# Performance work log

Measured on AMD Instinct MI355X. Metric: run time of the kernel, lower is better.

## Reference

```python
import jax, jax.numpy as jnp
import numpy as np

C = 112       # channels, divisible by NCHUNK
NCHUNK = 7    # shift_sizes[0]
PAD = 3       # shift_sizes[0] // 2
EPS = 1e-5


def _gn(x, g, b):
    # GroupNorm(1, C): normalize over (C, D, H, W) per sample, per-channel affine
    mu = jnp.mean(x, axis=(1, 2, 3, 4), keepdims=True)
    var = jnp.mean((x - mu) ** 2, axis=(1, 2, 3, 4), keepdims=True)
    xn = (x - mu) * jax.lax.rsqrt(var + EPS)
    return xn * g[None, :, None, None, None] + b[None, :, None, None, None]


def _conv1x1(x, w, b):
    # 1x1x1 Conv3d == channel-mixing GEMM
    return jnp.einsum('oc,bcdhw->bodhw', w, x) + b[None, :, None, None, None]


def _gelu(x):
    return jax.nn.gelu(x, approximate=False)  # torch nn.GELU default = exact erf


def _pad3(x):
    return jnp.pad(x, ((0, 0), (0, 0), (PAD, PAD), (PAD, PAD), (PAD, PAD)))


def _axial_shift(xp, axis, D, H, W):
    # chunk channels into NCHUNK groups, roll group i by (i - PAD) along `axis`,
    # concat, then narrow each spatial axis at offset PAD with ORIGINAL lengths
    chunks = jnp.split(xp, NCHUNK, axis=1)
    shifted = [jnp.roll(c, s, axis=axis) for c, s in zip(chunks, range(-PAD, PAD + 1))]
    xc = jnp.concatenate(shifted, axis=1)
    return xc[:, :, PAD:PAD + D, PAD:PAD + H, PAD:PAD + W]


def setup_inputs() -> dict:
    key = jax.random.key(0)
    ks = jax.random.split(key, 9)
    B, D, H, W = 1, 64, 64, 64
    hid = 4 * C

    def w(k, shape, fan_in):
        return jax.random.normal(k, shape, jnp.float32) * np.float32(1.0 / np.sqrt(fan_in))

    return {
        'x': jax.random.normal(ks[0], (B, C, D, H, W), jnp.float32),
        'conv1_w': w(ks[1], (C, C), C), 'conv1_b': jnp.zeros((C,), jnp.float32),
        'conv2d_w': w(ks[2], (C, C), C), 'conv2d_b': jnp.zeros((C,), jnp.float32),
        'conv2h_w': w(ks[3], (C, C), C), 'conv2h_b': jnp.zeros((C,), jnp.float32),
        'conv2w_w': w(ks[4], (C, C), C), 'conv2w_b': jnp.zeros((C,), jnp.float32),
        'conv3_w': w(ks[5], (C, C), C), 'conv3_b': jnp.zeros((C,), jnp.float32),
        'fc1_w': w(ks[6], (hid, C), C), 'fc1_b': jnp.zeros((hid,), jnp.float32),
        'fc2_w': w(ks[7], (C, hid), hid), 'fc2_b': jnp.zeros((C,), jnp.float32),
        'n1_g': jnp.ones((C,), jnp.float32), 'n1_b': jnp.zeros((C,), jnp.float32),
        'na1_g': jnp.ones((C,), jnp.float32), 'na1_b': jnp.zeros((C,), jnp.float32),
        'na2_g': jnp.ones((C,), jnp.float32), 'na2_b': jnp.zeros((C,), jnp.float32),
        'n2_g': jnp.ones((C,), jnp.float32), 'n2_b': jnp.zeros((C,), jnp.float32),
    }


def reference(x, conv1_w, conv1_b, conv2d_w, conv2d_b, conv2h_w, conv2h_b,
              conv2w_w, conv2w_b, conv3_w, conv3_b, fc1_w, fc1_b, fc2_w, fc2_b,
              n1_g, n1_b, na1_g, na1_b, na2_g, na2_b, n2_g, n2_b):
    B, _, D, H, W = x.shape
    shortcut = x
    h0 = _gn(x, n1_g, n1_b)                                   # block norm1

    # ---- AxialShift.axial_shift_single_scale ----
    a = _gelu(_gn(_conv1x1(h0, conv1_w, conv1_b), na1_g, na1_b))
    xp = _pad3(a)                                             # padded once (D branch)
    x_d = _gelu(_conv1x1(_axial_shift(xp, 2, D, H, W), conv2d_w, conv2d_b))
    xp = _pad3(xp)                                            # padded twice (H branch, as in source)
    x_h = _gelu(_conv1x1(_axial_shift(xp, 3, D, H, W), conv2h_w, conv2h_b))
    xp = _pad3(xp)                                            # padded thrice (W branch)
    x_w = _gelu(_conv1x1(_axial_shift(xp, 4, D, H, W), conv2w_w, conv2w_b))
    y = _conv1x1(_gn(x_d + x_h + x_w, na2_g, na2_b), conv3_w, conv3_b)
    y = y + h0                                                # AxialShift residual (x_masked == 0)

    x1 = shortcut + y                                         # block residual 1
    m = _gn(x1, n2_g, n2_b)                                   # block norm2
    m = _conv1x1(_gelu(_conv1x1(m, fc1_w, fc1_b)), fc2_w, fc2_b)  # Mlp (drop=0)
    return x1 + m
```

## Files before the change

### kernel.cpp

```cpp
#include <hip/hip_runtime.h>
#include <math.h>

static constexpr int CH   = 112;
static constexpr int HID  = 448;
static constexpr int NPOS = 64 * 64 * 64;
static constexpr long long NELEM = (long long)CH * NPOS;

typedef _Float16 f16x8 __attribute__((ext_vector_type(8)));
typedef _Float16 f16x4 __attribute__((ext_vector_type(4)));
typedef float    f32x4 __attribute__((ext_vector_type(4)));

__device__ __forceinline__ float gelu_f(float x) {
    return 0.5f * x * (1.0f + erff(x * 0.70710678118654752f));
}

__device__ __forceinline__ void stats_from(const double* __restrict__ S, float* mu, float* inv) {
    double m = S[0] / (double)NELEM;
    double v = S[1] / (double)NELEM - m * m;
    *mu  = (float)m;
    *inv = (float)(1.0 / sqrt(v + 1e-5));
}

__device__ __forceinline__ void block_reduce2(double s, double q, double* __restrict__ out) {
    #pragma unroll
    for (int off = 32; off > 0; off >>= 1) {
        s += __shfl_down(s, off, 64);
        q += __shfl_down(q, off, 64);
    }
    __shared__ double red[16];
    int lane = threadIdx.x & 63, wv = threadIdx.x >> 6;
    int nw = blockDim.x >> 6;
    if (lane == 0) { red[wv] = s; red[wv + 8] = q; }
    __syncthreads();
    if (threadIdx.x == 0) {
        double S = 0, Q = 0;
        for (int i = 0; i < nw; i++) { S += red[i]; Q += red[i + 8]; }
        atomicAdd(out, S);
        atomicAdd(out + 1, Q);
    }
}

__device__ __forceinline__ void mfma_tile(const _Float16* __restrict__ w,
                                          const _Float16 (*lsT)[136],
                                          int l15, int l4, int wv, f32x4 acc[7]) {
    #pragma unroll
    for (int kk = 0; kk < 4; kk++) {
        f16x8 b = *(const f16x8*)(&lsT[wv * 16 + l15][kk * 32 + l4 * 8]);
        #pragma unroll
        for (int mt = 0; mt < 7; mt++) {
            f16x8 a = *(const f16x8*)(w + (mt * 16 + l15) * 128 + kk * 32 + l4 * 8);
            acc[mt] = __builtin_amdgcn_mfma_f32_16x16x32_f16(a, b, acc[mt], 0, 0, 0);
        }
    }
}

__device__ __forceinline__ void accum_gelu(f32x4 tot[7], const f32x4 acc[7],
                                           const float* __restrict__ b, int l4) {
    #pragma unroll
    for (int mt = 0; mt < 7; mt++) {
        float4 bb = *(const float4*)(b + mt * 16 + l4 * 4);
        tot[mt][0] += gelu_f(acc[mt][0] + bb.x);
        tot[mt][1] += gelu_f(acc[mt][1] + bb.y);
        tot[mt][2] += gelu_f(acc[mt][2] + bb.z);
        tot[mt][3] += gelu_f(acc[mt][3] + bb.w);
    }
}

__global__ void k_reduce(const float* __restrict__ x, double* __restrict__ S) {
    long long i0 = (long long)blockIdx.x * blockDim.x + threadIdx.x;
    long long stride = (long long)gridDim.x * blockDim.x;
    const float4* x4 = (const float4*)x;
    long long n4 = NELEM / 4;
    double s = 0, q = 0;
    for (long long i = i0; i < n4; i += stride) {
        float4 v = x4[i];
        s += (double)v.x + (double)v.y + (double)v.z + (double)v.w;
        q += (double)v.x * v.x + (double)v.y * v.y + (double)v.z * v.z + (double)v.w * v.w;
    }
    block_reduce2(s, q, S);
}

__global__ void k_fold(const double* __restrict__ S, const float* __restrict__ w,
                       const float* __restrict__ b, const float* __restrict__ g,
                       const float* __restrict__ bta,
                       _Float16* __restrict__ w16, float* __restrict__ beff) {
    int o = blockIdx.x;
    float mu, inv; stats_from(S, &mu, &inv);
    float partial = 0.f;
    for (int c = threadIdx.x; c < 128; c += blockDim.x) {
        float wv_ = 0.f, contrib = 0.f;
        if (c < CH) {
            float sc = inv * g[c];
            float sh = bta[c] - mu * sc;
            float w0 = w[o * CH + c];
            wv_ = w0 * sc;
            contrib = w0 * sh;
        }
        w16[o * 128 + c] = (_Float16)wv_;
        partial += contrib;
    }
    #pragma unroll
    for (int off = 32; off > 0; off >>= 1) partial += __shfl_down(partial, off, 64);
    __shared__ float rp[2];
    int lane = threadIdx.x & 63, wv_ = threadIdx.x >> 6;
    if (lane == 0) rp[wv_] = partial;
    __syncthreads();
    if (threadIdx.x == 0) beff[o] = b[o] + rp[0] + rp[1];
}

__global__ void k_cast(const float* __restrict__ w2d, const float* __restrict__ w2h,
                       const float* __restrict__ w2w, const float* __restrict__ fc2w,
                       _Float16* __restrict__ w2dh, _Float16* __restrict__ w2hh,
                       _Float16* __restrict__ w2wh, _Float16* __restrict__ fc2h) {
    int b = blockIdx.x;
    if (b < CH) {
        for (int c = threadIdx.x; c < 128; c += blockDim.x) {
            float vd = 0.f, vh = 0.f, vw = 0.f;
            if (c < CH) { vd = w2d[b * CH + c]; vh = w2h[b * CH + c]; vw = w2w[b * CH + c]; }
            w2dh[b * 128 + c] = (_Float16)vd;
            w2hh[b * 128 + c] = (_Float16)vh;
            w2wh[b * 128 + c] = (_Float16)vw;
        }
    }
    for (int i = threadIdx.x; i < CH; i += blockDim.x)
        fc2h[b * CH + i] = (_Float16)fc2w[b * CH + i];
}

__global__ void __launch_bounds__(256, 2)
k_conv1(const float* __restrict__ x, const _Float16* __restrict__ w1h,
        const float* __restrict__ b1e, _Float16* __restrict__ t16, double* __restrict__ S1) {
    __shared__ __align__(16) _Float16 lxT[64][136];
    int tid = threadIdx.x, lane = tid & 63, wv = tid >> 6, l15 = lane & 15, l4 = lane >> 4;
    int pos0 = blockIdx.x * 64;

    {
        int c0 = tid >> 4, q = tid & 15;
        #pragma unroll
        for (int p = 0; p < 7; p++) {
            int c = p * 16 + c0;
            float4 v = *(const float4*)(x + (long long)c * NPOS + pos0 + q * 4);
            lxT[q * 4 + 0][c] = (_Float16)v.x;
            lxT[q * 4 + 1][c] = (_Float16)v.y;
            lxT[q * 4 + 2][c] = (_Float16)v.z;
            lxT[q * 4 + 3][c] = (_Float16)v.w;
        }
        for (int i = tid; i < 64 * 16; i += 256) lxT[i >> 4][112 + (i & 15)] = (_Float16)0.f;
    }
    __syncthreads();

    f32x4 acc[7];
    {
        f32x4 z = {0.f, 0.f, 0.f, 0.f};
        #pragma unroll
        for (int mt = 0; mt < 7; mt++) acc[mt] = z;
    }
    mfma_tile(w1h, lxT, l15, l4, wv, acc);

    long long posw = pos0 + wv * 16 + l15;
    double s = 0, q = 0;
    #pragma unroll
    for (int mt = 0; mt < 7; mt++) {
        int ob = mt * 16 + l4 * 4;
        float4 bb = *(const float4*)(b1e + ob);
        const float* bp = (const float*)&bb;
        f16x4 o4;
        #pragma unroll
        for (int r = 0; r < 4; r++) {
            float tv = acc[mt][r] + bp[r];
            o4[r] = (_Float16)tv;
            s += (double)tv; q += (double)tv * tv;
        }
        *(f16x4*)(t16 + posw * 128 + ob) = o4;
    }
    {
        f16x4 z4; z4[0] = z4[1] = z4[2] = z4[3] = (_Float16)0.f;
        *(f16x4*)(t16 + posw * 128 + 112 + l4 * 4) = z4;
    }
    block_reduce2(s, q, S1);
}

__global__ void k_act(const _Float16* __restrict__ t16, _Float16* __restrict__ a16,
                      const double* __restrict__ S1, const float* __restrict__ g,
                      const float* __restrict__ bta) {
    float mu, inv; stats_from(S1, &mu, &inv);
    long long i8 = (long long)blockIdx.x * blockDim.x + threadIdx.x;
    int c = (int)((i8 * 8) & 127);
    f16x8 r;
    if (c < 112) {
        f16x8 v = *(const f16x8*)(t16 + i8 * 8);
        float4 g0 = *(const float4*)(g + c);
        float4 g1 = *(const float4*)(g + c + 4);
        float4 b0 = *(const float4*)(bta + c);
        float4 b1 = *(const float4*)(bta + c + 4);
        const float* gp0 = (const float*)&g0; const float* gp1 = (const float*)&g1;
        const float* bp0 = (const float*)&b0; const float* bp1 = (const float*)&b1;
        #pragma unroll
        for (int j = 0; j < 4; j++) {
            float sc = inv * gp0[j], sh = bp0[j] - mu * sc;
            r[j] = (_Float16)gelu_f((float)v[j] * sc + sh);
        }
        #pragma unroll
        for (int j = 0; j < 4; j++) {
            float sc = inv * gp1[j], sh = bp1[j] - mu * sc;
            r[4 + j] = (_Float16)gelu_f((float)v[4 + j] * sc + sh);
        }
    } else {
        #pragma unroll
        for (int j = 0; j < 8; j++) r[j] = (_Float16)0.f;
    }
    *(f16x8*)(a16 + i8 * 8) = r;
}

__global__ void __launch_bounds__(256, 2)
k_shift(const _Float16* __restrict__ a16,
        const _Float16* __restrict__ w2dh, const float* __restrict__ b2d,
        const _Float16* __restrict__ w2hh, const float* __restrict__ b2h,
        const _Float16* __restrict__ w2wh, const float* __restrict__ b2w,
        _Float16* __restrict__ s16, double* __restrict__ S2) {
    __shared__ __align__(16) _Float16 lsT[64][136];
    int tid = threadIdx.x, lane = tid & 63, wv = tid >> 6, l15 = lane & 15, l4 = lane >> 4;
    int d = blockIdx.x >> 6, h = blockIdx.x & 63;

    f32x4 tot[7], acc[7];
    {
        f32x4 z = {0.f, 0.f, 0.f, 0.f};
        #pragma unroll
        for (int mt = 0; mt < 7; mt++) tot[mt] = z;
    }
    f16x8 z8;
    #pragma unroll
    for (int j = 0; j < 8; j++) z8[j] = (_Float16)0.f;

    for (int u = tid; u < 1024; u += 256) {
        int w = u >> 4, u16 = u & 15;
        f16x8 v = z8;
        if (u16 < 14) {
            int p = u16 >> 1;
            int dd = d - (p - 3);
            if ((unsigned)dd < 64u)
                v = *(const f16x8*)(a16 + (long long)(dd * 4096 + h * 64 + w) * 128 + u16 * 8);
        }
        *(f16x8*)(&lsT[w][u16 * 8]) = v;
    }
    __syncthreads();
    {
        f32x4 z = {0.f, 0.f, 0.f, 0.f};
        #pragma unroll
        for (int mt = 0; mt < 7; mt++) acc[mt] = z;
    }
    mfma_tile(w2dh, lsT, l15, l4, wv, acc);
    accum_gelu(tot, acc, b2d, l4);
    __syncthreads();

    {
        int dd = d - 3;
        bool dok = (unsigned)dd < 64u;
        for (int u = tid; u < 1024; u += 256) {
            int w = u >> 4, u16 = u & 15;
            f16x8 v = z8;
            if (u16 < 14) {
                int p = u16 >> 1;
                int hh = h - p;
                int ww = w - 3;
                if (dok && (unsigned)hh < 64u && ww >= 0)
                    v = *(const f16x8*)(a16 + (long long)(dd * 4096 + hh * 64 + ww) * 128 + u16 * 8);
            }
            *(f16x8*)(&lsT[w][u16 * 8]) = v;
        }
    }
    __syncthreads();
    {
        f32x4 z = {0.f, 0.f, 0.f, 0.f};
        #pragma unroll
        for (int mt = 0; mt < 7; mt++) acc[mt] = z;
    }
    mfma_tile(w2hh, lsT, l15, l4, wv, acc);
    accum_gelu(tot, acc, b2h, l4);
    __syncthreads();

    {
        int dd = d - 6, hh = h - 6;
        bool ok = ((unsigned)dd < 64u) && ((unsigned)hh < 64u);
        for (int u = tid; u < 1024; u += 256) {
            int w = u >> 4, u16 = u & 15;
            f16x8 v = z8;
            if (ok && u16 < 14) {
                int p = u16 >> 1;
                int ww = w - 3 - p;
                if ((unsigned)ww < 64u)
                    v = *(const f16x8*)(a16 + (long long)(dd * 4096 + hh * 64 + ww) * 128 + u16 * 8);
            }
            *(f16x8*)(&lsT[w][u16 * 8]) = v;
        }
    }
    __syncthreads();
    {
        f32x4 z = {0.f, 0.f, 0.f, 0.f};
        #pragma unroll
        for (int mt = 0; mt < 7; mt++) acc[mt] = z;
    }
    mfma_tile(w2wh, lsT, l15, l4, wv, acc);
    accum_gelu(tot, acc, b2w, l4);

    long long posw = d * 4096 + h * 64 + wv * 16 + l15;
    double s = 0, q = 0;
    #pragma unroll
    for (int mt = 0; mt < 7; mt++) {
        f16x4 o4;
        #pragma unroll
        for (int r = 0; r < 4; r++) {
            float sv = tot[mt][r];
            o4[r] = (_Float16)sv;
            s += (double)sv; q += (double)sv * sv;
        }
        *(f16x4*)(s16 + posw * 128 + mt * 16 + l4 * 4) = o4;
    }
    {
        f16x4 z4; z4[0] = z4[1] = z4[2] = z4[3] = (_Float16)0.f;
        *(f16x4*)(s16 + posw * 128 + 112 + l4 * 4) = z4;
    }
    block_reduce2(s, q, S2);
}

__global__ void __launch_bounds__(256, 2)
k_comb(const _Float16* __restrict__ s16, const float* __restrict__ x,
       const _Float16* __restrict__ w3h, const float* __restrict__ b3e,
       const double* __restrict__ S0, const float* __restrict__ n1g,
       const float* __restrict__ n1b, float* __restrict__ x1, double* __restrict__ S3) {
    __shared__ __align__(16) _Float16 lsT[64][136];
    int tid = threadIdx.x, lane = tid & 63, wv = tid >> 6, l15 = lane & 15, l4 = lane >> 4;
    int pos0 = blockIdx.x * 64;

    for (int u = tid; u < 1024; u += 256) {
        int w = u >> 4, u16 = u & 15;
        *(f16x8*)(&lsT[w][u16 * 8]) =
            *(const f16x8*)(s16 + (long long)(pos0 + w) * 128 + u16 * 8);
    }
    __syncthreads();

    f32x4 acc[7];
    {
        f32x4 z = {0.f, 0.f, 0.f, 0.f};
        #pragma unroll
        for (int mt = 0; mt < 7; mt++) acc[mt] = z;
    }
    mfma_tile(w3h, lsT, l15, l4, wv, acc);

    float mu, inv; stats_from(S0, &mu, &inv);
    long long posw = pos0 + wv * 16 + l15;
    double s = 0, q = 0;
    #pragma unroll
    for (int mt = 0; mt < 7; mt++) {
        int ob = mt * 16 + l4 * 4;
        float4 b3 = *(const float4*)(b3e + ob);
        float4 g4 = *(const float4*)(n1g + ob);
        float4 n4 = *(const float4*)(n1b + ob);
        const float* b3p = (const float*)&b3;
        const float* g4p = (const float*)&g4;
        const float* n4p = (const float*)&n4;
        #pragma unroll
        for (int r = 0; r < 4; r++) {
            int o = ob + r;
            float y  = acc[mt][r] + b3p[r];
            float xv = x[(long long)o * NPOS + posw];
            float sc = inv * g4p[r];
            float h0 = xv * sc + (n4p[r] - mu * sc);
            float v  = xv + y + h0;
            x1[(long long)o * NPOS + posw] = v;
            s += (double)v; q += (double)v * v;
        }
    }
    block_reduce2(s, q, S3);
}

__global__ void __launch_bounds__(256, 2)
k_mlp(float* __restrict__ x1out, const _Float16* __restrict__ fc1h,
      const float* __restrict__ b1m, const _Float16* __restrict__ fc2h,
      const float* __restrict__ fc2b) {
    __shared__ __align__(16) _Float16 lxT[64][136];
    __shared__ __align__(16) _Float16 GT[64][456];
    int tid  = threadIdx.x;
    int lane = tid & 63;
    int wv   = tid >> 6;
    int l15  = lane & 15;
    int l4   = lane >> 4;
    int pos0 = blockIdx.x * 64;

    {
        int c0 = tid >> 4;
        int q  = tid & 15;
        #pragma unroll
        for (int p = 0; p < 7; p++) {
            int c = p * 16 + c0;
            float4 v = *(const float4*)(x1out + (long long)c * NPOS + pos0 + q * 4);
            lxT[q * 4 + 0][c] = (_Float16)v.x;
            lxT[q * 4 + 1][c] = (_Float16)v.y;
            lxT[q * 4 + 2][c] = (_Float16)v.z;
            lxT[q * 4 + 3][c] = (_Float16)v.w;
        }
        for (int i = tid; i < 64 * 16; i += 256) {
            lxT[i >> 4][112 + (i & 15)] = (_Float16)0.f;
        }
    }
    __syncthreads();

    int hb = wv * 112;
    f32x4 acc1[7][4];
    {
        f32x4 z = {0.f, 0.f, 0.f, 0.f};
        #pragma unroll
        for (int mt = 0; mt < 7; mt++)
            #pragma unroll
            for (int nt = 0; nt < 4; nt++) acc1[mt][nt] = z;
    }
    #pragma unroll
    for (int kk = 0; kk < 4; kk++) {
        f16x8 a[7];
        #pragma unroll
        for (int mt = 0; mt < 7; mt++)
            a[mt] = *(const f16x8*)(fc1h + (hb + mt * 16 + l15) * 128 + kk * 32 + l4 * 8);
        #pragma unroll
        for (int nt = 0; nt < 4; nt++) {
            f16x8 b = *(const f16x8*)(&lxT[nt * 16 + l15][kk * 32 + l4 * 8]);
            #pragma unroll
            for (int mt = 0; mt < 7; mt++)
                acc1[mt][nt] = __builtin_amdgcn_mfma_f32_16x16x32_f16(a[mt], b, acc1[mt][nt], 0, 0, 0);
        }
    }
    #pragma unroll
    for (int mt = 0; mt < 7; mt++) {
        int hbase = hb + mt * 16 + l4 * 4;
        float4 bias = *(const float4*)(b1m + hbase);
        #pragma unroll
        for (int nt = 0; nt < 4; nt++) {
            f16x4 g4;
            g4[0] = (_Float16)gelu_f(acc1[mt][nt][0] + bias.x);
            g4[1] = (_Float16)gelu_f(acc1[mt][nt][1] + bias.y);
            g4[2] = (_Float16)gelu_f(acc1[mt][nt][2] + bias.z);
            g4[3] = (_Float16)gelu_f(acc1[mt][nt][3] + bias.w);
            *(f16x4*)(&GT[nt * 16 + l15][hbase]) = g4;
        }
    }
    __syncthreads();

    int pw = wv * 16 + l15;
    f32x4 acc2[7];
    {
        f32x4 z = {0.f, 0.f, 0.f, 0.f};
        #pragma unroll
        for (int mt = 0; mt < 7; mt++) acc2[mt] = z;
    }
    #pragma unroll 2
    for (int kk = 0; kk < 14; kk++) {
        f16x8 b = *(const f16x8*)(&GT[pw][kk * 32 + l4 * 8]);
        #pragma unroll
        for (int mt = 0; mt < 7; mt++) {
            f16x8 a = *(const f16x8*)(fc2h + (mt * 16 + l15) * 448 + kk * 32 + l4 * 8);
            acc2[mt] = __builtin_amdgcn_mfma_f32_16x16x32_f16(a, b, acc2[mt], 0, 0, 0);
        }
    }
    long long gp = pos0 + pw;
    #pragma unroll
    for (int mt = 0; mt < 7; mt++) {
        int ob = mt * 16 + l4 * 4;
        float4 b2 = *(const float4*)(fc2b + ob);
        float bb[4] = {b2.x, b2.y, b2.z, b2.w};
        #pragma unroll
        for (int r = 0; r < 4; r++) {
            long long idx = (long long)(ob + r) * NPOS + gp;
            x1out[idx] = x1out[idx] + acc2[mt][r] + bb[r];
        }
    }
}

extern "C" void kernel_launch(void* const* d_in, const int* in_sizes, int n_in,
                              void* d_out, int out_size, void* d_ws, size_t ws_size,
                              hipStream_t stream) {
    const float* x       = (const float*)d_in[0];
    const float* conv1_w = (const float*)d_in[1];
    const float* conv1_b = (const float*)d_in[2];
    const float* conv2d_w= (const float*)d_in[3];
    const float* conv2d_b= (const float*)d_in[4];
    const float* conv2h_w= (const float*)d_in[5];
    const float* conv2h_b= (const float*)d_in[6];
    const float* conv2w_w= (const float*)d_in[7];
    const float* conv2w_b= (const float*)d_in[8];
    const float* conv3_w = (const float*)d_in[9];
    const float* conv3_b = (const float*)d_in[10];
    const float* fc1_w   = (const float*)d_in[11];
    const float* fc1_b   = (const float*)d_in[12];
    const float* fc2_w   = (const float*)d_in[13];
    const float* fc2_b   = (const float*)d_in[14];
    const float* n1_g    = (const float*)d_in[15];
    const float* n1_b    = (const float*)d_in[16];
    const float* na1_g   = (const float*)d_in[17];
    const float* na1_b   = (const float*)d_in[18];
    const float* na2_g   = (const float*)d_in[19];
    const float* na2_b   = (const float*)d_in[20];
    const float* n2_g    = (const float*)d_in[21];
    const float* n2_b    = (const float*)d_in[22];

    char* ws = (char*)d_ws;
    double* S = (double*)ws;
    float* b1e = (float*)(ws + 512);
    float* b3e = b1e + 112;
    float* b1m = b3e + 112;
    _Float16* w1h  = (_Float16*)(ws + 3200);
    _Float16* w3h  = w1h  + 112 * 128;
    _Float16* w2dh = w3h  + 112 * 128;
    _Float16* w2hh = w2dh + 112 * 128;
    _Float16* w2wh = w2hh + 112 * 128;
    _Float16* fc1h = w2wh + 112 * 128;
    _Float16* fc2h = fc1h + 448 * 128;
    float* bufA = (float*)(ws + (1 << 20));
    _Float16* t16 = (_Float16*)bufA;
    _Float16* s16 = (_Float16*)bufA;
    float* out  = (float*)d_out;
    _Float16* a16 = (_Float16*)out;

    hipMemsetAsync(S, 0, 8 * sizeof(double), stream);
    k_cast<<<448, 128, 0, stream>>>(conv2d_w, conv2h_w, conv2w_w, fc2_w,
                                    w2dh, w2hh, w2wh, fc2h);
    k_reduce<<<1024, 256, 0, stream>>>(x, S);
    k_fold<<<112, 128, 0, stream>>>(S, conv1_w, conv1_b, n1_g, n1_b, w1h, b1e);
    k_conv1<<<4096, 256, 0, stream>>>(x, w1h, b1e, t16, S + 2);
    k_act<<<16384, 256, 0, stream>>>(t16, a16, S + 2, na1_g, na1_b);
    k_shift<<<4096, 256, 0, stream>>>(a16, w2dh, conv2d_b, w2hh, conv2h_b,
                                      w2wh, conv2w_b, s16, S + 4);
    k_fold<<<112, 128, 0, stream>>>(S + 4, conv3_w, conv3_b, na2_g, na2_b, w3h, b3e);
    k_comb<<<4096, 256, 0, stream>>>(s16, x, w3h, b3e, S, n1_g, n1_b, out, S + 6);
    k_fold<<<448, 128, 0, stream>>>(S + 6, fc1_w, fc1_b, n2_g, n2_b, fc1h, b1m);
    k_mlp<<<4096, 256, 0, stream>>>(out, fc1h, b1m, fc2h, fc2_b);
}
```

Measured before the change: 1.201 ms.

## Cut MLP shared memory via two-phase GT staging and fp16 x1 copy

k_comb now also writes an fp16 position-major copy of x1 into the scratch buffer, so k_mlp can load its input tile with vectorized row copies instead of transposing fp32 channel-major data. k_mlp reuses a single smaller shared buffer: the GELU outputs are kept in registers and written into shared memory in two halves, each consumed by half of the fc2 K loop. This shrinks LDS use so launch bounds allow three blocks per CU. The erf in GELU is also replaced by a polynomial approximation (Abramowitz-Stegun form) using a hardware reciprocal and exp2, which changes accuracy slightly; the extra registers held for g16 could cause spills.

```diff
diff --git a/kernel.cpp b/kernel.cpp
--- a/kernel.cpp
+++ b/kernel.cpp
@@ -11,7 +11,14 @@
 typedef float    f32x4 __attribute__((ext_vector_type(4)));
 
 __device__ __forceinline__ float gelu_f(float x) {
-    return 0.5f * x * (1.0f + erff(x * 0.70710678118654752f));
+    float ax = fabsf(x) * 0.70710678118654752f;
+    float t  = __builtin_amdgcn_rcpf(1.0f + 0.3275911f * ax);
+    float p  = t * (0.254829592f + t * (-0.284496736f + t * (1.421413741f +
+               t * (-1.453152027f + t * 1.061405429f))));
+    float e  = exp2f(-1.4426950408889634f * ax * ax);
+    float er = 1.0f - p * e;
+    er = (x < 0.f) ? -er : er;
+    return 0.5f * x * (1.0f + er);
 }
 
 __device__ __forceinline__ void stats_from(const double* __restrict__ S, float* mu, float* inv) {
@@ -323,10 +330,11 @@
 }
 
 __global__ void __launch_bounds__(256, 2)
-k_comb(const _Float16* __restrict__ s16, const float* __restrict__ x,
+k_comb(const _Float16* s16, const float* __restrict__ x,
        const _Float16* __restrict__ w3h, const float* __restrict__ b3e,
        const double* __restrict__ S0, const float* __restrict__ n1g,
-       const float* __restrict__ n1b, float* __restrict__ x1, double* __restrict__ S3) {
+       const float* __restrict__ n1b, float* __restrict__ x1,
+       _Float16* x1h, double* __restrict__ S3) {
     __shared__ __align__(16) _Float16 lsT[64][136];
     int tid = threadIdx.x, lane = tid & 63, wv = tid >> 6, l15 = lane & 15, l4 = lane >> 4;
     int pos0 = blockIdx.x * 64;
@@ -358,6 +366,7 @@
         const float* b3p = (const float*)&b3;
         const float* g4p = (const float*)&g4;
         const float* n4p = (const float*)&n4;
+        f16x4 o4;
         #pragma unroll
         for (int r = 0; r < 4; r++) {
             int o = ob + r;
@@ -367,40 +376,28 @@
             float h0 = xv * sc + (n4p[r] - mu * sc);
             float v  = xv + y + h0;
             x1[(long long)o * NPOS + posw] = v;
+            o4[r] = (_Float16)v;
             s += (double)v; q += (double)v * v;
         }
+        *(f16x4*)(x1h + posw * 128 + ob) = o4;
     }
     block_reduce2(s, q, S3);
 }
 
-__global__ void __launch_bounds__(256, 2)
-k_mlp(float* __restrict__ x1out, const _Float16* __restrict__ fc1h,
-      const float* __restrict__ b1m, const _Float16* __restrict__ fc2h,
-      const float* __restrict__ fc2b) {
-    __shared__ __align__(16) _Float16 lxT[64][136];
-    __shared__ __align__(16) _Float16 GT[64][456];
-    int tid  = threadIdx.x;
-    int lane = tid & 63;
-    int wv   = tid >> 6;
-    int l15  = lane & 15;
-    int l4   = lane >> 4;
+__global__ void __launch_bounds__(256, 3)
+k_mlp(float* __restrict__ x1out, const _Float16* __restrict__ x1h,
+      const _Float16* __restrict__ fc1h, const float* __restrict__ b1m,
+      const _Float16* __restrict__ fc2h, const float* __restrict__ fc2b) {
+    __shared__ __align__(16) char smem[64 * 232 * 2];
+    _Float16 (*lxT)[136] = (_Float16 (*)[136])smem;
+    _Float16 (*GT)[232]  = (_Float16 (*)[232])smem;
+    int tid = threadIdx.x, lane = tid & 63, wv = tid >> 6, l15 = lane & 15, l4 = lane >> 4;
     int pos0 = blockIdx.x * 64;
 
-    {
-        int c0 = tid >> 4;
-        int q  = tid & 15;
-        #pragma unroll
-        for (int p = 0; p < 7; p++) {
-            int c = p * 16 + c0;
-            float4 v = *(const float4*)(x1out + (long long)c * NPOS + pos0 + q * 4);
-            lxT[q * 4 + 0][c] = (_Float16)v.x;
-            lxT[q * 4 + 1][c] = (_Float16)v.y;
-            lxT[q * 4 + 2][c] = (_Float16)v.z;
-            lxT[q * 4 + 3][c] = (_Float16)v.w;
-        }
-        for (int i = tid; i < 64 * 16; i += 256) {
-            lxT[i >> 4][112 + (i & 15)] = (_Float16)0.f;
-        }
+    for (int u = tid; u < 1024; u += 256) {
+        int w = u >> 4, u16 = u & 15;
+        *(f16x8*)(&lxT[w][u16 * 8]) =
+            *(const f16x8*)(x1h + (long long)(pos0 + w) * 128 + u16 * 8);
     }
     __syncthreads();
 
@@ -427,18 +424,16 @@
                 acc1[mt][nt] = __builtin_amdgcn_mfma_f32_16x16x32_f16(a[mt], b, acc1[mt][nt], 0, 0, 0);
         }
     }
+    f16x4 g16[7][4];
     #pragma unroll
     for (int mt = 0; mt < 7; mt++) {
-        int hbase = hb + mt * 16 + l4 * 4;
-        float4 bias = *(const float4*)(b1m + hbase);
+        float4 bias = *(const float4*)(b1m + hb + mt * 16 + l4 * 4);
         #pragma unroll
         for (int nt = 0; nt < 4; nt++) {
-            f16x4 g4;
-            g4[0] = (_Float16)gelu_f(acc1[mt][nt][0] + bias.x);
-            g4[1] = (_Float16)gelu_f(acc1[mt][nt][1] + bias.y);
-            g4[2] = (_Float16)gelu_f(acc1[mt][nt][2] + bias.z);
-            g4[3] = (_Float16)gelu_f(acc1[mt][nt][3] + bias.w);
-            *(f16x4*)(&GT[nt * 16 + l15][hbase]) = g4;
+            g16[mt][nt][0] = (_Float16)gelu_f(acc1[mt][nt][0] + bias.x);
+            g16[mt][nt][1] = (_Float16)gelu_f(acc1[mt][nt][1] + bias.y);
+            g16[mt][nt][2] = (_Float16)gelu_f(acc1[mt][nt][2] + bias.z);
+            g16[mt][nt][3] = (_Float16)gelu_f(acc1[mt][nt][3] + bias.w);
         }
     }
     __syncthreads();
@@ -450,15 +445,31 @@
         #pragma unroll
         for (int mt = 0; mt < 7; mt++) acc2[mt] = z;
     }
-    #pragma unroll 2
-    for (int kk = 0; kk < 14; kk++) {
-        f16x8 b = *(const f16x8*)(&GT[pw][kk * 32 + l4 * 8]);
-        #pragma unroll
-        for (int mt = 0; mt < 7; mt++) {
-            f16x8 a = *(const f16x8*)(fc2h + (mt * 16 + l15) * 448 + kk * 32 + l4 * 8);
-            acc2[mt] = __builtin_amdgcn_mfma_f32_16x16x32_f16(a, b, acc2[mt], 0, 0, 0);
-        }
-    }
+    #pragma unroll
+    for (int ph = 0; ph < 2; ph++) {
+        if ((wv >> 1) == ph) {
+            int cb = (wv & 1) * 112;
+            #pragma unroll
+            for (int mt = 0; mt < 7; mt++) {
+                int col = cb + mt * 16 + l4 * 4;
+                #pragma unroll
+                for (int nt = 0; nt < 4; nt++)
+                    *(f16x4*)(&GT[nt * 16 + l15][col]) = g16[mt][nt];
+            }
+        }
+        __syncthreads();
+        #pragma unroll
+        for (int kk = 0; kk < 7; kk++) {
+            f16x8 b = *(const f16x8*)(&GT[pw][kk * 32 + l4 * 8]);
+            #pragma unroll
+            for (int mt = 0; mt < 7; mt++) {
+                f16x8 a = *(const f16x8*)(fc2h + (mt * 16 + l15) * 448 + ph * 224 + kk * 32 + l4 * 8);
+                acc2[mt] = __builtin_amdgcn_mfma_f32_16x16x32_f16(a, b, acc2[mt], 0, 0, 0);
+            }
+        }
+        if (ph == 0) __syncthreads();
+    }
+
     long long gp = pos0 + pw;
     #pragma unroll
     for (int mt = 0; mt < 7; mt++) {
@@ -515,6 +526,7 @@
     float* bufA = (float*)(ws + (1 << 20));
     _Float16* t16 = (_Float16*)bufA;
     _Float16* s16 = (_Float16*)bufA;
+    _Float16* x1h = (_Float16*)bufA;
     float* out  = (float*)d_out;
     _Float16* a16 = (_Float16*)out;
 
@@ -528,7 +540,7 @@
     k_shift<<<4096, 256, 0, stream>>>(a16, w2dh, conv2d_b, w2hh, conv2h_b,
                                       w2wh, conv2w_b, s16, S + 4);
     k_fold<<<112, 128, 0, stream>>>(S + 4, conv3_w, conv3_b, na2_g, na2_b, w3h, b3e);
-    k_comb<<<4096, 256, 0, stream>>>(s16, x, w3h, b3e, S, n1_g, n1_b, out, S + 6);
+    k_comb<<<4096, 256, 0, stream>>>(s16, x, w3h, b3e, S, n1_g, n1_b, out, x1h, S + 6);
     k_fold<<<448, 128, 0, stream>>>(S + 6, fc1_w, fc1_b, n2_g, n2_b, fc1h, b1m);
-    k_mlp<<<4096, 256, 0, stream>>>(out, fc1h, b1m, fc2h, fc2_b);
-}
+    k_mlp<<<4096, 256, 0, stream>>>(out, x1h, fc1h, b1m, fc2h, fc2_b);
+}
```

Result: faster. 1.126 ms (-6.3%).
